# Optimization experiments

Hardware: AMD Instinct MI355X
Metric: run time of the kernel (lower is better)

Reference implementation:

```python
import jax, jax.numpy as jnp
import numpy as np

NEG_BIG = -1.0e9


def setup_inputs() -> dict:
    key = jax.random.key(0)
    ks = jax.random.split(key, 6)
    B, H, L, D = 2, 16, 2048, 64
    q = jax.random.normal(ks[0], (B, H, L, D), dtype=jnp.float32)
    k = jax.random.normal(ks[1], (B, H, L, D), dtype=jnp.float32)
    v = jax.random.normal(ks[2], (B, H, L, D), dtype=jnp.float32)
    p_q = jax.random.normal(ks[3], (B, L, 3), dtype=jnp.float32)
    p_k = jax.random.normal(ks[4], (B, L, 3), dtype=jnp.float32)
    mask = jax.random.randint(ks[5], (B, L), 0, 2, dtype=jnp.int32)
    return {"q": q, "k": k, "v": v, "p_q": p_q, "p_k": p_k, "mask": mask}


def reference(q, k, v, p_q, p_k, mask):
    # learned score function instantiated as scaled dot-product: [B,H,Lq,Lk]
    d_head = q.shape[-1]
    scores = jnp.einsum("bhqd,bhkd->bhqk", q, k) / jnp.sqrt(jnp.float32(d_head))
    # mask: [B, Lk] -> [B, 1, 1, Lk]; additive -1e9 on masked keys
    m = mask.astype(scores.dtype)[:, None, None, :]
    scores = scores + m * NEG_BIG
    # softplus normalization (instead of softmax), scaled by key length v.shape[2]
    Lk = v.shape[2]
    scores = jax.nn.softplus(scores) / Lk
    out = jnp.einsum("bhqk,bhkd->bhqd", scores, v)
    return (out, scores)
```

## Files before the change

kernel.cpp:

```cpp
#include <hip/hip_runtime.h>

typedef float f32x4  __attribute__((ext_vector_type(4)));
typedef float f32x16 __attribute__((ext_vector_type(16)));
typedef short s16x8  __attribute__((ext_vector_type(8)));
typedef unsigned short u16;

#define LL 2048
#define DD 64
#define NITER 32
#define SC_OFF 4194304ull

struct SMem {
    u16 Khi[2][64][72];
    u16 VT [2][64][72];
    union {
        u16 Q[128][72];
        unsigned char P[4][4096];
    } u;
};

__device__ __forceinline__ u16 bf16_rne(float x) {
    unsigned u = __builtin_bit_cast(unsigned, x);
    return (u16)((u + 0x7FFFu + ((u >> 16) & 1u)) >> 16);
}
__device__ __forceinline__ float bf16f(u16 h) {
    unsigned u = (unsigned)h << 16;
    return __builtin_bit_cast(float, u);
}

__global__ __launch_bounds__(512, 4)
void psam_kernel(const float* __restrict__ Qg0, const float* __restrict__ Kg0,
                 const float* __restrict__ Vg0, const int* __restrict__ Mg0,
                 float* __restrict__ out)
{
    __shared__ SMem sm;
    const int tid = threadIdx.x;
    const int w = tid >> 6, l = tid & 63;
    const int j31 = l & 31, h = l >> 5;
    const int cw = w & 1, iw = w >> 1;
    const int cwj = cw * 32 + j31;
    const int colb = cwj * 2;

    const int bid = ((int)blockIdx.x & 7) * 64 + ((int)blockIdx.x >> 3);
    const int bh = bid >> 4;
    const int m0 = (bid & 15) << 7;
    const int bB = bh >> 4;

    const float* Qg = Qg0 + ((size_t)bh * LL + m0) * DD;
    const float* Kg = Kg0 + (size_t)bh * LL * DD;
    const float* Vg = Vg0 + (size_t)bh * LL * DD;
    const int*   Mg = Mg0 + (size_t)bB * LL;
    float* So = out + SC_OFF + (size_t)bh * LL * LL + (size_t)m0 * LL;
    float* Oo = out + ((size_t)bh * LL + m0) * DD;

    const int qi = tid >> 2, qd = (tid & 3) * 16;
    f32x4 qv[4];
    {
        const f32x4* s = (const f32x4*)(Qg + qi * DD + qd);
        qv[0] = s[0]; qv[1] = s[1]; qv[2] = s[2]; qv[3] = s[3];
    }
    u16 qhi16[16];
#pragma unroll
    for (int e = 0; e < 16; ++e) qhi16[e] = bf16_rne(qv[e >> 2][e & 3]);
    {
        s16x8 a, b;
#pragma unroll
        for (int i = 0; i < 8; ++i) { a[i] = (short)qhi16[i]; b[i] = (short)qhi16[8 + i]; }
        *(s16x8*)&sm.u.Q[qi][qd] = a;
        *(s16x8*)&sm.u.Q[qi][qd + 8] = b;
    }
    __syncthreads();
    s16x8 qfh[4], qfl[4];
#pragma unroll
    for (int ks = 0; ks < 4; ++ks)
        qfh[ks] = *(const s16x8*)&sm.u.Q[iw * 32 + j31][ks * 16 + h * 8];
    __syncthreads();
    {
        s16x8 a, b;
#pragma unroll
        for (int i = 0; i < 8; ++i) {
            a[i] = (short)bf16_rne(qv[i >> 2][i & 3] - bf16f(qhi16[i]));
            b[i] = (short)bf16_rne(qv[(8 + i) >> 2][(8 + i) & 3] - bf16f(qhi16[8 + i]));
        }
        *(s16x8*)&sm.u.Q[qi][qd] = a;
        *(s16x8*)&sm.u.Q[qi][qd + 8] = b;
    }
    __syncthreads();
#pragma unroll
    for (int ks = 0; ks < 4; ++ks)
        qfl[ks] = *(const s16x8*)&sm.u.Q[iw * 32 + j31][ks * 16 + h * 8];

    const int kc = tid >> 3, kd = (tid & 7) * 8;
    const int vc = tid & 63, vd = (tid >> 6) * 8;
    f32x4 kvx, kvy, vvx, vvy;
    {
        const f32x4* s = (const f32x4*)(Kg + (size_t)kc * DD + kd);
        kvx = s[0]; kvy = s[1];
        const f32x4* s2 = (const f32x4*)(Vg + (size_t)vc * DD + vd);
        vvx = s2[0]; vvy = s2[1];
    }
    {
        s16x8 kv;
#pragma unroll
        for (int i = 0; i < 4; ++i) { kv[i] = (short)bf16_rne(kvx[i]); kv[4 + i] = (short)bf16_rne(kvy[i]); }
        *(s16x8*)&sm.Khi[0][kc][kd] = kv;
#pragma unroll
        for (int i = 0; i < 4; ++i) {
            sm.VT[0][vd + i][vc]     = bf16_rne(vvx[i]);
            sm.VT[0][vd + 4 + i][vc] = bf16_rne(vvy[i]);
        }
    }
    {
        const f32x4* s = (const f32x4*)(Kg + (size_t)(64 + kc) * DD + kd);
        kvx = s[0]; kvy = s[1];
        const f32x4* s2 = (const f32x4*)(Vg + (size_t)(64 + vc) * DD + vd);
        vvx = s2[0]; vvy = s2[1];
    }
    float blc = -1.0e9f * (float)Mg[cwj];
    float bln = -1.0e9f * (float)Mg[64 + cwj];

    f32x16 accO;
#pragma unroll
    for (int e = 0; e < 16; ++e) accO[e] = 0.0f;

    unsigned char* spw = &sm.u.P[iw][0];
    __syncthreads();

    int buf = 0;
    for (int t = 0; t < NITER; ++t) {
        const int j0 = t * 64;

        f32x16 accS;
#pragma unroll
        for (int e = 0; e < 16; ++e) accS[e] = 0.0f;
#pragma unroll
        for (int ks = 0; ks < 4; ++ks) {
            s16x8 kf = *(const s16x8*)&sm.Khi[buf][cwj][ks * 16 + h * 8];
            accS = __builtin_amdgcn_mfma_f32_32x32x16_bf16(qfh[ks], kf, accS, 0, 0, 0);
            accS = __builtin_amdgcn_mfma_f32_32x32x16_bf16(qfl[ks], kf, accS, 0, 0, 0);
        }
        const float bl = blc;
        float* sp = So + (size_t)(iw * 32 + 4 * h) * LL + j0 + cwj;
#pragma unroll
        for (int g = 0; g < 4; ++g) {
#pragma unroll
            for (int r = 0; r < 4; ++r) {
                float x  = accS[g * 4 + r] * 0.125f + bl;
                float tt = __builtin_amdgcn_exp2f(x * 1.44269504f);
                float p  = __builtin_amdgcn_logf(1.0f + tt) * 3.38450771757785852e-4f;
                __builtin_nontemporal_store(p, sp + (size_t)(8 * g + r) * LL);
                const int il = 8 * g + 4 * h + r;
                *(u16*)(spw + ((il * 128 + colb) ^ ((il & 7) << 4))) = bf16_rne(p);
            }
        }
        asm volatile("s_waitcnt lgkmcnt(0)" ::: "memory");
        __builtin_amdgcn_s_barrier();

#pragma unroll
        for (int ks = 0; ks < 4; ++ks) {
            s16x8 va = *(const s16x8*)&sm.VT[buf][cwj][ks * 16 + h * 8];
            s16x8 pb = *(const s16x8*)(spw + ((j31 * 128 + ks * 32 + h * 16) ^ ((j31 & 7) << 4)));
            accO = __builtin_amdgcn_mfma_f32_32x32x16_bf16(va, pb, accO, 0, 0, 0);
        }

        if (t + 1 < NITER) {
            s16x8 kv;
#pragma unroll
            for (int i = 0; i < 4; ++i) { kv[i] = (short)bf16_rne(kvx[i]); kv[4 + i] = (short)bf16_rne(kvy[i]); }
            *(s16x8*)&sm.Khi[buf ^ 1][kc][kd] = kv;
#pragma unroll
            for (int i = 0; i < 4; ++i) {
                sm.VT[buf ^ 1][vd + i][vc]     = bf16_rne(vvx[i]);
                sm.VT[buf ^ 1][vd + 4 + i][vc] = bf16_rne(vvy[i]);
            }
        }
        {
            const int tp = (t + 2 < NITER) ? (t + 2) : (NITER - 1);
            const f32x4* s1 = (const f32x4*)(Kg + (size_t)(tp * 64 + kc) * DD + kd);
            kvx = s1[0]; kvy = s1[1];
            const f32x4* s2 = (const f32x4*)(Vg + (size_t)(tp * 64 + vc) * DD + vd);
            vvx = s2[0]; vvy = s2[1];
            blc = bln;
            bln = -1.0e9f * (float)Mg[tp * 64 + cwj];
        }
        asm volatile("s_waitcnt lgkmcnt(0)" ::: "memory");
        __builtin_amdgcn_s_barrier();
        buf ^= 1;
    }

#pragma unroll
    for (int g = 0; g < 4; ++g) {
        f32x4 o;
#pragma unroll
        for (int r = 0; r < 4; ++r) o[r] = accO[g * 4 + r];
        *(f32x4*)(Oo + (size_t)(iw * 32 + j31) * DD + cw * 32 + h * 4 + g * 8) = o;
    }
}

extern "C" void kernel_launch(void* const* d_in, const int* in_sizes, int n_in,
                              void* d_out, int out_size, void* d_ws, size_t ws_size,
                              hipStream_t stream) {
    const float* q    = (const float*)d_in[0];
    const float* k    = (const float*)d_in[1];
    const float* v    = (const float*)d_in[2];
    const int*   mask = (const int*)d_in[5];
    float* out = (float*)d_out;
    hipLaunchKernelGGL(psam_kernel, dim3(512), dim3(512), 0, stream, q, k, v, mask, out);
}
```

Before: 139.3 us.

## Split P·V over key halves per wave to drop mid-loop barrier

Each wave now writes its own 32x32 probability tile into a private LDS slot and immediately computes a partial P·V over its 32 keys for all 64 output dims, using two accumulators. The per-iteration barrier between the score write and the P·V read is removed, and the two column-wave partials are summed through LDS at the end. Q fragments are now loaded straight from global memory and split into bf16 hi/lo in registers, which removes the staging round trips through LDS and their barriers. In exchange the kernel holds more accumulator registers, issues twice as many VT loads, and adds a final cross-wave reduction.

After: 148.5 us. 1.07x slower.

```diff
diff --git a/kernel.cpp b/kernel.cpp
--- a/kernel.cpp
+++ b/kernel.cpp
@@ -13,10 +13,7 @@
 struct SMem {
     u16 Khi[2][64][72];
     u16 VT [2][64][72];
-    union {
-        u16 Q[128][72];
-        unsigned char P[4][4096];
-    } u;
+    u16 P  [8][1024];
 };
 
 __device__ __forceinline__ u16 bf16_rne(float x) {
@@ -39,56 +36,36 @@
     const int j31 = l & 31, h = l >> 5;
     const int cw = w & 1, iw = w >> 1;
     const int cwj = cw * 32 + j31;
-    const int colb = cwj * 2;
 
     const int bid = ((int)blockIdx.x & 7) * 64 + ((int)blockIdx.x >> 3);
     const int bh = bid >> 4;
     const int m0 = (bid & 15) << 7;
     const int bB = bh >> 4;
 
-    const float* Qg = Qg0 + ((size_t)bh * LL + m0) * DD;
     const float* Kg = Kg0 + (size_t)bh * LL * DD;
     const float* Vg = Vg0 + (size_t)bh * LL * DD;
     const int*   Mg = Mg0 + (size_t)bB * LL;
     float* So = out + SC_OFF + (size_t)bh * LL * LL + (size_t)m0 * LL;
     float* Oo = out + ((size_t)bh * LL + m0) * DD;
 
-    const int qi = tid >> 2, qd = (tid & 3) * 16;
-    f32x4 qv[4];
-    {
-        const f32x4* s = (const f32x4*)(Qg + qi * DD + qd);
-        qv[0] = s[0]; qv[1] = s[1]; qv[2] = s[2]; qv[3] = s[3];
-    }
-    u16 qhi16[16];
-#pragma unroll
-    for (int e = 0; e < 16; ++e) qhi16[e] = bf16_rne(qv[e >> 2][e & 3]);
-    {
-        s16x8 a, b;
-#pragma unroll
-        for (int i = 0; i < 8; ++i) { a[i] = (short)qhi16[i]; b[i] = (short)qhi16[8 + i]; }
-        *(s16x8*)&sm.u.Q[qi][qd] = a;
-        *(s16x8*)&sm.u.Q[qi][qd + 8] = b;
-    }
-    __syncthreads();
     s16x8 qfh[4], qfl[4];
-#pragma unroll
-    for (int ks = 0; ks < 4; ++ks)
-        qfh[ks] = *(const s16x8*)&sm.u.Q[iw * 32 + j31][ks * 16 + h * 8];
-    __syncthreads();
-    {
-        s16x8 a, b;
-#pragma unroll
-        for (int i = 0; i < 8; ++i) {
-            a[i] = (short)bf16_rne(qv[i >> 2][i & 3] - bf16f(qhi16[i]));
-            b[i] = (short)bf16_rne(qv[(8 + i) >> 2][(8 + i) & 3] - bf16f(qhi16[8 + i]));
-        }
-        *(s16x8*)&sm.u.Q[qi][qd] = a;
-        *(s16x8*)&sm.u.Q[qi][qd + 8] = b;
-    }
-    __syncthreads();
-#pragma unroll
-    for (int ks = 0; ks < 4; ++ks)
-        qfl[ks] = *(const s16x8*)&sm.u.Q[iw * 32 + j31][ks * 16 + h * 8];
+    {
+        const float* qr = Qg0 + ((size_t)bh * LL + m0 + iw * 32 + j31) * DD + h * 8;
+#pragma unroll
+        for (int ks = 0; ks < 4; ++ks) {
+            f32x4 a = *(const f32x4*)(qr + ks * 16);
+            f32x4 b = *(const f32x4*)(qr + ks * 16 + 4);
+#pragma unroll
+            for (int i = 0; i < 4; ++i) {
+                u16 hi = bf16_rne(a[i]);
+                qfh[ks][i] = (short)hi;
+                qfl[ks][i] = (short)bf16_rne(a[i] - bf16f(hi));
+                hi = bf16_rne(b[i]);
+                qfh[ks][4 + i] = (short)hi;
+                qfl[ks][4 + i] = (short)bf16_rne(b[i] - bf16f(hi));
+            }
+        }
+    }
 
     const int kc = tid >> 3, kd = (tid & 7) * 8;
     const int vc = tid & 63, vd = (tid >> 6) * 8;
@@ -119,12 +96,13 @@
     float blc = -1.0e9f * (float)Mg[cwj];
     float bln = -1.0e9f * (float)Mg[64 + cwj];
 
-    f32x16 accO;
-#pragma unroll
-    for (int e = 0; e < 16; ++e) accO[e] = 0.0f;
-
-    unsigned char* spw = &sm.u.P[iw][0];
-    __syncthreads();
+    f32x16 accO0, accO1;
+#pragma unroll
+    for (int e = 0; e < 16; ++e) { accO0[e] = 0.0f; accO1[e] = 0.0f; }
+
+    char* spw = (char*)&sm.P[w][0];
+    asm volatile("s_waitcnt lgkmcnt(0)" ::: "memory");
+    __builtin_amdgcn_s_barrier();
 
     int buf = 0;
     for (int t = 0; t < NITER; ++t) {
@@ -149,18 +127,18 @@
                 float tt = __builtin_amdgcn_exp2f(x * 1.44269504f);
                 float p  = __builtin_amdgcn_logf(1.0f + tt) * 3.38450771757785852e-4f;
                 __builtin_nontemporal_store(p, sp + (size_t)(8 * g + r) * LL);
-                const int il = 8 * g + 4 * h + r;
-                *(u16*)(spw + ((il * 128 + colb) ^ ((il & 7) << 4))) = bf16_rne(p);
-            }
-        }
-        asm volatile("s_waitcnt lgkmcnt(0)" ::: "memory");
-        __builtin_amdgcn_s_barrier();
-
-#pragma unroll
-        for (int ks = 0; ks < 4; ++ks) {
-            s16x8 va = *(const s16x8*)&sm.VT[buf][cwj][ks * 16 + h * 8];
-            s16x8 pb = *(const s16x8*)(spw + ((j31 * 128 + ks * 32 + h * 16) ^ ((j31 & 7) << 4)));
-            accO = __builtin_amdgcn_mfma_f32_32x32x16_bf16(va, pb, accO, 0, 0, 0);
+                const int q = 8 * g + 4 * h + r;
+                *(u16*)(spw + q * 64 + ((j31 * 2) ^ ((q & 3) << 4))) = bf16_rne(p);
+            }
+        }
+
+#pragma unroll
+        for (int ks2 = 0; ks2 < 2; ++ks2) {
+            s16x8 pb = *(const s16x8*)(spw + j31 * 64 + ((ks2 * 32 + h * 16) ^ ((j31 & 3) << 4)));
+            s16x8 va0 = *(const s16x8*)&sm.VT[buf][j31][cw * 32 + ks2 * 16 + h * 8];
+            accO0 = __builtin_amdgcn_mfma_f32_32x32x16_bf16(va0, pb, accO0, 0, 0, 0);
+            s16x8 va1 = *(const s16x8*)&sm.VT[buf][32 + j31][cw * 32 + ks2 * 16 + h * 8];
+            accO1 = __builtin_amdgcn_mfma_f32_32x32x16_bf16(va1, pb, accO1, 0, 0, 0);
         }
 
         if (t + 1 < NITER) {
@@ -188,12 +166,37 @@
         buf ^= 1;
     }
 
-#pragma unroll
-    for (int g = 0; g < 4; ++g) {
-        f32x4 o;
-#pragma unroll
-        for (int r = 0; r < 4; ++r) o[r] = accO[g * 4 + r];
-        *(f32x4*)(Oo + (size_t)(iw * 32 + j31) * DD + cw * 32 + h * 4 + g * 8) = o;
+    float* red = (float*)&sm;
+    if (cw == 1) {
+#pragma unroll
+        for (int db = 0; db < 2; ++db) {
+            const f32x16& a = db ? accO1 : accO0;
+#pragma unroll
+            for (int g = 0; g < 4; ++g)
+#pragma unroll
+                for (int r = 0; r < 4; ++r) {
+                    const int row = db * 32 + 8 * g + 4 * h + r;
+                    red[(size_t)(iw * 64 + row) * 32 + j31] = a[g * 4 + r];
+                }
+        }
+    }
+    __syncthreads();
+    if (cw == 0) {
+        float* op = Oo + (size_t)(iw * 32 + j31) * DD;
+#pragma unroll
+        for (int db = 0; db < 2; ++db) {
+            const f32x16& a = db ? accO1 : accO0;
+#pragma unroll
+            for (int g = 0; g < 4; ++g) {
+                f32x4 o;
+#pragma unroll
+                for (int r = 0; r < 4; ++r) {
+                    const int row = db * 32 + 8 * g + 4 * h + r;
+                    o[r] = a[g * 4 + r] + red[(size_t)(iw * 64 + row) * 32 + j31];
+                }
+                *(f32x4*)(op + db * 32 + 8 * g + 4 * h) = o;
+            }
+        }
     }
 }
 
```
